# Kernel optimization log

Hardware: AMD Instinct MI355X
Metric: run time of the kernel (lower is better)

The kernel has to match this reference:

```python
import jax, jax.numpy as jnp
import numpy as np

N_HEADS = 16
ROPE_BASE = 10000.0


def _rotate_half(x):
    d = x.shape[-1] // 2
    return jnp.concatenate([-x[..., d:], x[..., :d]], axis=-1)


def _rope_tables(L, head_dim, dtype):
    inv_freq = 1.0 / (ROPE_BASE ** (jnp.arange(0, head_dim, 2, dtype=jnp.float32) / head_dim))
    t = jnp.arange(L, dtype=jnp.float32)
    freqs = jnp.outer(t, inv_freq)  # [L, head_dim//2]
    # torch code repeats cos/sin along last dim (tile x2) -> concat([c, c])
    cos = jnp.concatenate([jnp.cos(freqs), jnp.cos(freqs)], axis=-1).astype(dtype)
    sin = jnp.concatenate([jnp.sin(freqs), jnp.sin(freqs)], axis=-1).astype(dtype)
    return cos[None, None], sin[None, None]  # [1,1,L,head_dim]


def setup_inputs() -> dict:
    key = jax.random.key(0)
    kx, kq, kk, kv, ko = jax.random.split(key, 5)
    B, L, D = 4, 2048, 1024
    s = 0.02
    return {
        "x": jax.random.normal(kx, (B, L, D), dtype=jnp.float32),
        "Wq": jax.random.normal(kq, (D, D), dtype=jnp.float32) * s,
        "Wk": jax.random.normal(kk, (D, D), dtype=jnp.float32) * s,
        "Wv": jax.random.normal(kv, (D, D), dtype=jnp.float32) * s,
        "Wo": jax.random.normal(ko, (D, D), dtype=jnp.float32) * s,
    }


def reference(x, Wq, Wk, Wv, Wo):
    B, L, D = x.shape
    H = N_HEADS
    hd = D // H

    def split_heads(y):
        return y.reshape(B, L, H, hd).transpose(0, 2, 1, 3)  # [B,H,L,hd]

    q = split_heads(x @ Wq.T)
    k = split_heads(x @ Wk.T)
    v = split_heads(x @ Wv.T)

    cos, sin = _rope_tables(L, hd, x.dtype)
    q = q * cos + _rotate_half(q) * sin
    k = k * cos + _rotate_half(k) * sin

    scale = 1.0 / jnp.sqrt(jnp.asarray(hd, dtype=x.dtype))
    scores = jnp.einsum("bhqd,bhkd->bhqk", q, k) * scale
    attn = jax.nn.softmax(scores, axis=-1)
    out = jnp.einsum("bhqk,bhkd->bhqd", attn, v)
    out = out.transpose(0, 2, 1, 3).reshape(B, L, D)
    return out @ Wo.T
```

## Files before the change

kernel.cpp:

```cpp
#include <hip/hip_runtime.h>


typedef __bf16 bf16_t;
typedef __bf16 bf16x8 __attribute__((ext_vector_type(8)));
typedef __bf16 bf16x4 __attribute__((ext_vector_type(4)));
typedef float  floatx4 __attribute__((ext_vector_type(4)));

#define B_  4
#define L_  2048
#define D_  1024
#define H_  16
#define HD_ 64
#define M_  (B_*L_)

__device__ __forceinline__ void async_copy16(const bf16_t* g, bf16_t* l) {
  __builtin_amdgcn_global_load_lds(
      (const __attribute__((address_space(1))) void*)g,
      (__attribute__((address_space(3))) void*)l, 16, 0, 0);
}

__device__ __forceinline__ unsigned int pack_bf16(float a, float b) {
  unsigned short ua = __builtin_bit_cast(unsigned short, (bf16_t)a);
  unsigned short ub = __builtin_bit_cast(unsigned short, (bf16_t)b);
  return (unsigned int)ua | ((unsigned int)ub << 16);
}

__global__ void prep_kernel(const float* __restrict__ x,
                            const float* __restrict__ wq, const float* __restrict__ wk,
                            const float* __restrict__ wv, const float* __restrict__ wo,
                            bf16_t* __restrict__ xb,
                            bf16_t* __restrict__ wqb, bf16_t* __restrict__ wkb,
                            bf16_t* __restrict__ wvb, bf16_t* __restrict__ wob,
                            float* __restrict__ cosT, float* __restrict__ sinT)
{
  const int NX = M_*D_;
  const int NW = D_*D_;
  int i = blockIdx.x*256 + threadIdx.x;
  if (i < NX) { xb[i] = (bf16_t)x[i]; return; }
  i -= NX;
  if (i < NW) { wqb[i] = (bf16_t)wq[i]; return; }
  i -= NW;
  if (i < NW) { wkb[i] = (bf16_t)wk[i]; return; }
  i -= NW;
  if (i < NW) { wvb[i] = (bf16_t)wv[i]; return; }
  i -= NW;
  if (i < NW) { wob[i] = (bf16_t)wo[i]; return; }
  i -= NW;
  if (i < L_*32) {
    int l = i >> 5, f = i & 31;
    double inv = pow(10000.0, -(double)f / 32.0);
    double ang = (double)l * inv;
    cosT[i] = (float)cos(ang);
    sinT[i] = (float)sin(ang);
  }
}

template<int MODE>
__global__ __launch_bounds__(256) void gemm_kernel(
    const bf16_t* __restrict__ A,
    const bf16_t* __restrict__ W0, const bf16_t* __restrict__ W1, const bf16_t* __restrict__ W2,
    bf16_t* __restrict__ C0, bf16_t* __restrict__ C1, bf16_t* __restrict__ C2,
    float* __restrict__ Cf,
    const float* __restrict__ cosT, const float* __restrict__ sinT)
{
  __shared__ __align__(16) bf16_t As[128*64];
  __shared__ __align__(16) bf16_t Bs[128*64];
  const int KD = 1024, ND = 1024;
  int z = (MODE==0) ? (int)blockIdx.z : 0;
  const bf16_t* W = (MODE==1) ? W0 : (z==0 ? W0 : (z==1 ? W1 : W2));
  int m0 = blockIdx.y*128, n0 = blockIdx.x*128;
  int tid = threadIdx.x;
  int wave = tid>>6, lane = tid&63, quad = lane>>4, lr = lane&15;
  int wm = wave>>1, wn = wave&1;
  int srow = lane>>3, sslot = lane&7;

  floatx4 zero4 = {0.f,0.f,0.f,0.f};
  floatx4 acc[4][4];
  #pragma unroll
  for (int i=0;i<4;i++)
    #pragma unroll
    for (int j=0;j<4;j++) acc[i][j] = zero4;

  #pragma unroll 1
  for (int k0 = 0; k0 < KD; k0 += 64) {
    #pragma unroll
    for (int j=0;j<4;j++) {
      int chunk = wave + j*4;
      int row = chunk*8 + srow;
      int col = ((sslot ^ (row&7)) << 3);
      async_copy16(A + (size_t)(m0+row)*KD + k0 + col, &As[chunk*512]);
      async_copy16(W + (size_t)(n0+row)*KD + k0 + col, &Bs[chunk*512]);
    }
    __syncthreads();
    #pragma unroll
    for (int ks=0; ks<2; ks++) {
      bf16x8 af[4], bfr[4];
      #pragma unroll
      for (int mi=0;mi<4;mi++)
        af[mi] = *(const bf16x8*)&As[(wm*64+mi*16+lr)*64 + (((ks*4+quad) ^ (lr&7))<<3)];
      #pragma unroll
      for (int ni=0;ni<4;ni++)
        bfr[ni] = *(const bf16x8*)&Bs[(wn*64+ni*16+lr)*64 + (((ks*4+quad) ^ (lr&7))<<3)];
      #pragma unroll
      for (int mi=0;mi<4;mi++)
        #pragma unroll
        for (int ni=0;ni<4;ni++)
          acc[mi][ni] = __builtin_amdgcn_mfma_f32_16x16x32_bf16(af[mi], bfr[ni], acc[mi][ni], 0,0,0);
    }
    __syncthreads();
  }

  if (MODE==1) {
    #pragma unroll
    for (int mi=0;mi<4;mi++) {
      int row = m0 + wm*64 + mi*16 + quad*4;
      #pragma unroll
      for (int ni=0;ni<4;ni++) {
        int col = n0 + wn*64 + ni*16 + lr;
        #pragma unroll
        for (int r=0;r<4;r++)
          Cf[(size_t)(row+r)*ND + col] = acc[mi][ni][r];
      }
    }
  } else if (z < 2) {
    bf16_t* Cb = (z==0) ? C0 : C1;
    const float sc = (z==0) ? 0.18033688011112042f : 1.0f;
    #pragma unroll
    for (int mi=0;mi<4;mi++) {
      int row = m0 + wm*64 + mi*16 + quad*4;
      int l = row & 2047;
      #pragma unroll
      for (int ni=0;ni<2;ni++) {
        int col = n0 + wn*64 + ni*16 + lr;
        int f = ni*16 + lr;
        #pragma unroll
        for (int r=0;r<4;r++) {
          float c = cosT[(l+r)*32 + f];
          float s = sinT[(l+r)*32 + f];
          float lo = acc[mi][ni][r], hi = acc[mi][ni+2][r];
          Cb[(size_t)(row+r)*ND + col]      = (bf16_t)((lo*c - hi*s)*sc);
          Cb[(size_t)(row+r)*ND + col + 32] = (bf16_t)((hi*c + lo*s)*sc);
        }
      }
    }
  } else {
    #pragma unroll
    for (int mi=0;mi<4;mi++) {
      int row0 = m0 + wm*64 + mi*16 + quad*4;
      int bb = row0 >> 11, ll = row0 & 2047;
      #pragma unroll
      for (int ni=0;ni<4;ni++) {
        int col = n0 + wn*64 + ni*16 + lr;
        int hh = col >> 6, dd = col & 63;
        uint2 val;
        val.x = pack_bf16(acc[mi][ni][0], acc[mi][ni][1]);
        val.y = pack_bf16(acc[mi][ni][2], acc[mi][ni][3]);
        *(uint2*)&C2[((size_t)((bb<<4)+hh)*64 + dd)*2048 + ll] = val;
      }
    }
  }
}

__global__ __launch_bounds__(256) void attn_kernel(
    const bf16_t* __restrict__ Q, const bf16_t* __restrict__ K,
    const bf16_t* __restrict__ Vt, bf16_t* __restrict__ Op,
    float* __restrict__ Ls)
{
  __shared__ __align__(16) bf16_t Ks[2][2048];
  __shared__ __align__(16) bf16_t Vs[2][2048];
  __shared__ __align__(16) bf16_t Pl[8*640];
  int tid = threadIdx.x;
  int wave = tid>>6, lane = tid&63, quad = lane>>4, lr = lane&15;
  int bh = blockIdx.x; int b = bh>>4, h = bh&15;
  int z = blockIdx.z;
  int q0 = blockIdx.y*128 + wave*32;
  size_t rowQ = (size_t)b*L_ + q0;
  int kvbase = z*1024;

  int ksrow = wave*8 + (lane>>3);
  int kscol = (((lane&7) ^ (ksrow&7)) << 3);
  int vrow  = tid>>2;
  int vscol = (((lane&3) ^ (vrow&3)) << 3);

  bf16x8 qf[2][2];
  #pragma unroll
  for (int n=0;n<2;n++)
    #pragma unroll
    for (int ks=0;ks<2;ks++)
      qf[n][ks] = *(const bf16x8*)&Q[(rowQ + n*16 + lr)*D_ + h*HD_ + ks*32 + quad*8];

  const bf16_t* Kg = K + ((size_t)b*L_ + kvbase)*D_ + h*HD_;
  const bf16_t* Vg = Vt + ((size_t)bh*HD_)*L_ + kvbase;

  bf16_t* P0 = &Pl[(wave*2+0)*640];
  bf16_t* P1 = &Pl[(wave*2+1)*640];

  float lsum0 = 0.f, lsum1 = 0.f;
  floatx4 zero4 = {0.f,0.f,0.f,0.f};
  floatx4 accO[2][4];
  #pragma unroll
  for (int n=0;n<2;n++)
    #pragma unroll
    for (int dt=0;dt<4;dt++) accO[n][dt] = zero4;

  auto stage = [&](int it, int c) {
    async_copy16(Kg + (size_t)(it*32 + ksrow)*D_ + kscol, &Ks[c][wave*512]);
    async_copy16(Vg + (size_t)vrow*L_ + it*32 + vscol,    &Vs[c][wave*512]);
  };

  stage(0, 0);
  __syncthreads();

  #pragma unroll 1
  for (int it = 0; it < 32; ++it) {
    int c = it & 1;
    if (it < 31) stage(it+1, c^1);

    floatx4 St[2][2];
    St[0][0]=zero4; St[0][1]=zero4; St[1][0]=zero4; St[1][1]=zero4;
    #pragma unroll
    for (int t=0;t<2;t++) {
      #pragma unroll
      for (int ks=0;ks<2;ks++) {
        bf16x8 kf = *(const bf16x8*)&Ks[c][(t*16+lr)*64 + (((ks*4+quad) ^ (lr&7))<<3)];
        St[0][t] = __builtin_amdgcn_mfma_f32_16x16x32_bf16(kf, qf[0][ks], St[0][t], 0,0,0);
        St[1][t] = __builtin_amdgcn_mfma_f32_16x16x32_bf16(kf, qf[1][ks], St[1][t], 0,0,0);
      }
    }

    #pragma unroll
    for (int n=0;n<2;n++) {
      bf16_t* Pw = n ? P1 : P0;
      float ls = 0.f;
      #pragma unroll
      for (int t=0;t<2;t++) {
        float p0 = exp2f(St[n][t][0]), p1 = exp2f(St[n][t][1]);
        float p2 = exp2f(St[n][t][2]), p3 = exp2f(St[n][t][3]);
        ls += (p0+p1)+(p2+p3);
        uint2 w;
        w.x = pack_bf16(p0,p1); w.y = pack_bf16(p2,p3);
        *(uint2*)&Pw[lr*40 + t*16 + quad*4] = w;
      }
      if (n) lsum1 += ls; else lsum0 += ls;
    }

    bf16x8 pf0 = *(const bf16x8*)&P0[lr*40 + quad*8];
    bf16x8 pf1 = *(const bf16x8*)&P1[lr*40 + quad*8];
    #pragma unroll
    for (int dt=0;dt<4;dt++) {
      bf16x8 vf = *(const bf16x8*)&Vs[c][(dt*16+lr)*32 + (((quad) ^ (lr&3))<<3)];
      accO[0][dt] = __builtin_amdgcn_mfma_f32_16x16x32_bf16(vf, pf0, accO[0][dt], 0,0,0);
      accO[1][dt] = __builtin_amdgcn_mfma_f32_16x16x32_bf16(vf, pf1, accO[1][dt], 0,0,0);
    }

    __syncthreads();
  }

  lsum0 += __shfl_xor(lsum0, 16, 64);
  lsum0 += __shfl_xor(lsum0, 32, 64);
  lsum1 += __shfl_xor(lsum1, 16, 64);
  lsum1 += __shfl_xor(lsum1, 32, 64);

  bf16_t* Opz = Op + (size_t)z*M_*D_;
  #pragma unroll
  for (int n=0;n<2;n++) {
    #pragma unroll
    for (int dt=0;dt<4;dt++) {
      uint2 w;
      w.x = pack_bf16(accO[n][dt][0], accO[n][dt][1]);
      w.y = pack_bf16(accO[n][dt][2], accO[n][dt][3]);
      *(uint2*)&Opz[(rowQ + n*16 + lr)*D_ + h*HD_ + dt*16 + quad*4] = w;
    }
  }
  if (quad == 0) {
    Ls[z*131072 + bh*2048 + q0 + lr]      = lsum0;
    Ls[z*131072 + bh*2048 + q0 + 16 + lr] = lsum1;
  }
}

__global__ void reduce_kernel(const bf16_t* __restrict__ Op, const float* __restrict__ Ls,
                              bf16_t* __restrict__ O)
{
  int i = blockIdx.x*256 + threadIdx.x;
  size_t e = (size_t)i*4;
  int d  = (int)(e & 1023);
  int bl = (int)(e >> 10);
  int bq = bl >> 11, l = bl & 2047, h = d >> 6;
  int li = (bq*16 + h)*2048 + l;
  float inv = 1.0f / (Ls[li] + Ls[li + 131072]);
  bf16x4 v0 = *(const bf16x4*)&Op[e];
  bf16x4 v1 = *(const bf16x4*)&Op[(size_t)M_*D_ + e];
  bf16x4 r;
  #pragma unroll
  for (int j=0;j<4;j++)
    r[j] = (bf16_t)(((float)v0[j] + (float)v1[j]) * inv);
  *(bf16x4*)&O[e] = r;
}

extern "C" void kernel_launch(void* const* d_in, const int* in_sizes, int n_in,
                              void* d_out, int out_size, void* d_ws, size_t ws_size,
                              hipStream_t stream) {
  const float* x  = (const float*)d_in[0];
  const float* wq = (const float*)d_in[1];
  const float* wk = (const float*)d_in[2];
  const float* wv = (const float*)d_in[3];
  const float* wo = (const float*)d_in[4];

  char* ws = (char*)d_ws;
  bf16_t* xb  = (bf16_t*)(ws);
  bf16_t* Qb  = (bf16_t*)(ws + (size_t)(16u<<20));
  bf16_t* Kb  = (bf16_t*)(ws + (size_t)(32u<<20));
  bf16_t* Vtb = (bf16_t*)(ws + (size_t)(48u<<20));
  bf16_t* wqb = (bf16_t*)(ws + (size_t)(64u<<20));
  bf16_t* wkb = (bf16_t*)(ws + (size_t)(66u<<20));
  bf16_t* wvb = (bf16_t*)(ws + (size_t)(68u<<20));
  bf16_t* wob = (bf16_t*)(ws + (size_t)(70u<<20));
  float* cosT = (float*)(ws + (size_t)(72u<<20));
  float* sinT = (float*)(ws + (size_t)(72u<<20) + (256u<<10));
  float* Ls   = (float*)wqb;
  bf16_t* Opart = (bf16_t*)d_out;
  bf16_t* Ob = xb;

  prep_kernel<<<49408, 256, 0, stream>>>(x, wq, wk, wv, wo, xb, wqb, wkb, wvb, wob, cosT, sinT);
  gemm_kernel<0><<<dim3(8,64,3), 256, 0, stream>>>(xb, wqb, wkb, wvb, Qb, Kb, Vtb, nullptr, cosT, sinT);
  attn_kernel<<<dim3(64,16,2), 256, 0, stream>>>(Qb, Kb, Vtb, Opart, Ls);
  reduce_kernel<<<8192, 256, 0, stream>>>(Opart, Ls, Ob);
  gemm_kernel<1><<<dim3(8,64,1), 256, 0, stream>>>(Ob, wob, nullptr, nullptr,
                                                   nullptr, nullptr, nullptr, (float*)d_out, cosT, sinT);
}
```

Measured before the change: 332.0 us.

## Keep softmax probabilities in registers via permlane swap and compute row sums with MFMA

Drops the LDS round-trip for the P tile in the attention kernel. The K rows read from LDS are permuted and the V swizzle is changed so that exp2 results can be repacked straight into MFMA B-operand fragments using permlane32_swap. Row sums now come from an extra MFMA against a ones vector instead of scalar adds plus cross-lane shuffles, and s_setprio is placed around the MFMA sections. This removes LDS writes and reads and a dependency on LDS latency per iteration, but the row sums are now accumulated from bf16-rounded probabilities, which changes precision slightly.

```diff
diff --git a/kernel.cpp b/kernel.cpp
--- a/kernel.cpp
+++ b/kernel.cpp
@@ -5,6 +5,7 @@
 typedef __bf16 bf16x8 __attribute__((ext_vector_type(8)));
 typedef __bf16 bf16x4 __attribute__((ext_vector_type(4)));
 typedef float  floatx4 __attribute__((ext_vector_type(4)));
+typedef unsigned int u32x2 __attribute__((ext_vector_type(2)));
 
 #define B_  4
 #define L_  2048
@@ -168,7 +169,6 @@
 {
   __shared__ __align__(16) bf16_t Ks[2][2048];
   __shared__ __align__(16) bf16_t Vs[2][2048];
-  __shared__ __align__(16) bf16_t Pl[8*640];
   int tid = threadIdx.x;
   int wave = tid>>6, lane = tid&63, quad = lane>>4, lr = lane&15;
   int bh = blockIdx.x; int b = bh>>4, h = bh&15;
@@ -177,10 +177,13 @@
   size_t rowQ = (size_t)b*L_ + q0;
   int kvbase = z*1024;
 
+  int slr = (lr&3) | ((lr&4)<<1) | ((lr&8)>>1);
+  int vg  = ((lr>>2) ^ lr) & 3;
+
   int ksrow = wave*8 + (lane>>3);
   int kscol = (((lane&7) ^ (ksrow&7)) << 3);
   int vrow  = tid>>2;
-  int vscol = (((lane&3) ^ (vrow&3)) << 3);
+  int vscol = (((lane&3) ^ (((vrow>>2)^vrow)&3)) << 3);
 
   bf16x8 qf[2][2];
   #pragma unroll
@@ -192,12 +195,14 @@
   const bf16_t* Kg = K + ((size_t)b*L_ + kvbase)*D_ + h*HD_;
   const bf16_t* Vg = Vt + ((size_t)bh*HD_)*L_ + kvbase;
 
-  bf16_t* P0 = &Pl[(wave*2+0)*640];
-  bf16_t* P1 = &Pl[(wave*2+1)*640];
-
-  float lsum0 = 0.f, lsum1 = 0.f;
+  bf16x8 onesf;
+  #pragma unroll
+  for (int j=0;j<8;j++) onesf[j] = (bf16_t)1.0f;
+
   floatx4 zero4 = {0.f,0.f,0.f,0.f};
   floatx4 accO[2][4];
+  floatx4 accS[2];
+  accS[0] = zero4; accS[1] = zero4;
   #pragma unroll
   for (int n=0;n<2;n++)
     #pragma unroll
@@ -218,48 +223,45 @@
 
     floatx4 St[2][2];
     St[0][0]=zero4; St[0][1]=zero4; St[1][0]=zero4; St[1][1]=zero4;
+    __builtin_amdgcn_s_setprio(1);
     #pragma unroll
     for (int t=0;t<2;t++) {
       #pragma unroll
       for (int ks=0;ks<2;ks++) {
-        bf16x8 kf = *(const bf16x8*)&Ks[c][(t*16+lr)*64 + (((ks*4+quad) ^ (lr&7))<<3)];
+        bf16x8 kf = *(const bf16x8*)&Ks[c][(t*16+slr)*64 + (((ks*4+quad) ^ (slr&7))<<3)];
         St[0][t] = __builtin_amdgcn_mfma_f32_16x16x32_bf16(kf, qf[0][ks], St[0][t], 0,0,0);
         St[1][t] = __builtin_amdgcn_mfma_f32_16x16x32_bf16(kf, qf[1][ks], St[1][t], 0,0,0);
       }
     }
-
+    __builtin_amdgcn_s_setprio(0);
+
+    bf16x8 pfv[2];
     #pragma unroll
     for (int n=0;n<2;n++) {
-      bf16_t* Pw = n ? P1 : P0;
-      float ls = 0.f;
-      #pragma unroll
-      for (int t=0;t<2;t++) {
-        float p0 = exp2f(St[n][t][0]), p1 = exp2f(St[n][t][1]);
-        float p2 = exp2f(St[n][t][2]), p3 = exp2f(St[n][t][3]);
-        ls += (p0+p1)+(p2+p3);
-        uint2 w;
-        w.x = pack_bf16(p0,p1); w.y = pack_bf16(p2,p3);
-        *(uint2*)&Pw[lr*40 + t*16 + quad*4] = w;
-      }
-      if (n) lsum1 += ls; else lsum0 += ls;
-    }
-
-    bf16x8 pf0 = *(const bf16x8*)&P0[lr*40 + quad*8];
-    bf16x8 pf1 = *(const bf16x8*)&P1[lr*40 + quad*8];
+      unsigned int w00 = pack_bf16(exp2f(St[n][0][0]), exp2f(St[n][0][1]));
+      unsigned int w01 = pack_bf16(exp2f(St[n][0][2]), exp2f(St[n][0][3]));
+      unsigned int w10 = pack_bf16(exp2f(St[n][1][0]), exp2f(St[n][1][1]));
+      unsigned int w11 = pack_bf16(exp2f(St[n][1][2]), exp2f(St[n][1][3]));
+      u32x2 r0 = __builtin_amdgcn_permlane32_swap(w00, w10, false, false);
+      u32x2 r1 = __builtin_amdgcn_permlane32_swap(w01, w11, false, false);
+      union { unsigned int u[4]; bf16x8 v; } pu;
+      pu.u[0] = r0.x; pu.u[1] = r1.x; pu.u[2] = r0.y; pu.u[3] = r1.y;
+      pfv[n] = pu.v;
+    }
+
+    __builtin_amdgcn_s_setprio(1);
     #pragma unroll
     for (int dt=0;dt<4;dt++) {
-      bf16x8 vf = *(const bf16x8*)&Vs[c][(dt*16+lr)*32 + (((quad) ^ (lr&3))<<3)];
-      accO[0][dt] = __builtin_amdgcn_mfma_f32_16x16x32_bf16(vf, pf0, accO[0][dt], 0,0,0);
-      accO[1][dt] = __builtin_amdgcn_mfma_f32_16x16x32_bf16(vf, pf1, accO[1][dt], 0,0,0);
-    }
+      bf16x8 vf = *(const bf16x8*)&Vs[c][(dt*16+lr)*32 + ((quad ^ vg)<<3)];
+      accO[0][dt] = __builtin_amdgcn_mfma_f32_16x16x32_bf16(vf, pfv[0], accO[0][dt], 0,0,0);
+      accO[1][dt] = __builtin_amdgcn_mfma_f32_16x16x32_bf16(vf, pfv[1], accO[1][dt], 0,0,0);
+    }
+    accS[0] = __builtin_amdgcn_mfma_f32_16x16x32_bf16(onesf, pfv[0], accS[0], 0,0,0);
+    accS[1] = __builtin_amdgcn_mfma_f32_16x16x32_bf16(onesf, pfv[1], accS[1], 0,0,0);
+    __builtin_amdgcn_s_setprio(0);
 
     __syncthreads();
   }
-
-  lsum0 += __shfl_xor(lsum0, 16, 64);
-  lsum0 += __shfl_xor(lsum0, 32, 64);
-  lsum1 += __shfl_xor(lsum1, 16, 64);
-  lsum1 += __shfl_xor(lsum1, 32, 64);
 
   bf16_t* Opz = Op + (size_t)z*M_*D_;
   #pragma unroll
@@ -273,8 +275,8 @@
     }
   }
   if (quad == 0) {
-    Ls[z*131072 + bh*2048 + q0 + lr]      = lsum0;
-    Ls[z*131072 + bh*2048 + q0 + 16 + lr] = lsum1;
+    Ls[z*131072 + bh*2048 + q0 + lr]      = accS[0][0];
+    Ls[z*131072 + bh*2048 + q0 + 16 + lr] = accS[1][0];
   }
 }
 
```

Result: no change. 338.4 us (+1.9%).
